# Kernel optimization log

Measured on AMD Instinct MI355X. Metric: run time of the kernel, lower is better.

## Reference

```python
import jax, jax.numpy as jnp
import numpy as np

N, F_IN, HID, OUT, H = 10000, 256, 256, 512, 4
E = 320000
SLOPE = 0.2  # GATv2Conv default negative_slope
EPS = 1e-5   # LayerNorm eps


def setup_inputs() -> dict:
    key = jax.random.key(0)
    ks = jax.random.split(key, 10)
    g = lambda k, shape, fan: (jax.random.normal(k, shape, jnp.float32) / np.float32(np.sqrt(fan)))
    d1, d2 = HID // H, OUT // H
    return {
        "x": jax.random.normal(ks[0], (N, F_IN), jnp.float32),
        "edge_index": jax.random.randint(ks[1], (2, E), 0, N),
        # layer 1 (in_feats -> hidden_dim, heads=H, concat)
        "Wl1": g(ks[2], (HID, F_IN), F_IN), "bl1": jnp.zeros((HID,), jnp.float32),
        "Wr1": g(ks[3], (HID, F_IN), F_IN), "br1": jnp.zeros((HID,), jnp.float32),
        "att1": g(ks[4], (H, d1), d1), "bias1": jnp.zeros((HID,), jnp.float32),
        # layer 2 (hidden_dim -> out_dim)
        "Wl2": g(ks[5], (OUT, HID), HID), "bl2": jnp.zeros((OUT,), jnp.float32),
        "Wr2": g(ks[6], (OUT, HID), HID), "br2": jnp.zeros((OUT,), jnp.float32),
        "att2": g(ks[7], (H, d2), d2), "bias2": jnp.zeros((OUT,), jnp.float32),
        # final LayerNorm
        "gamma": jnp.ones((OUT,), jnp.float32), "beta": jnp.zeros((OUT,), jnp.float32),
    }


def _gatv2(x, src, dst, Wl, bl, Wr, br, att, bias, heads):
    """GATv2Conv: e_ij = a_h . leaky_relu(Wl x_j + Wr x_i), softmax over j per i,
    out_i = sum_j alpha_ij * (Wl x_j), heads concatenated, plus bias."""
    n = x.shape[0]
    d = Wl.shape[0] // heads
    xl = (x @ Wl.T + bl).reshape(n, heads, d)  # source transform
    xr = (x @ Wr.T + br).reshape(n, heads, d)  # target transform
    s = jax.nn.leaky_relu(xl[src] + xr[dst], SLOPE)        # [E,H,d]
    e = jnp.einsum('ehd,hd->eh', s, att)                   # [E,H]
    m = jax.ops.segment_max(e, dst, num_segments=n)        # [N,H] (self-loops => no empty segs)
    w = jnp.exp(e - m[dst])
    denom = jax.ops.segment_sum(w, dst, num_segments=n)
    alpha = w / denom[dst]                                 # segment softmax
    out = jax.ops.segment_sum(alpha[:, :, None] * xl[src], dst, num_segments=n)  # [N,H,d]
    return out.reshape(n, heads * d) + bias


def reference(x, edge_index, Wl1, bl1, Wr1, br1, att1, bias1,
              Wl2, bl2, Wr2, br2, att2, bias2, gamma, beta):
    n = x.shape[0]
    loop = jnp.arange(n, dtype=edge_index.dtype)  # add_self_loops=True
    src = jnp.concatenate([edge_index[0], loop])
    dst = jnp.concatenate([edge_index[1], loop])
    h = jax.nn.relu(_gatv2(x, src, dst, Wl1, bl1, Wr1, br1, att1, bias1, H))
    h = _gatv2(h, src, dst, Wl2, bl2, Wr2, br2, att2, bias2, H)
    mu = jnp.mean(h, axis=-1, keepdims=True)
    var = jnp.var(h, axis=-1, keepdims=True)
    return gamma * (h - mu) / jnp.sqrt(var + EPS) + beta
```

## Files before the change

kernel.cpp:

```cpp
#include <hip/hip_runtime.h>
#include <stdint.h>

#define N_NODES 10000
#define K_DIM   256
#define HID_D   256
#define OUT_D   512
#define NE      320000
#define NE_TOT  (NE + N_NODES)
#define SLOPE   0.2f
#define LN_EPS  1e-5f

typedef __bf16 bf16x8 __attribute__((ext_vector_type(8)));
typedef float  f32x4  __attribute__((ext_vector_type(4)));
typedef float  f32x2  __attribute__((ext_vector_type(2)));
typedef unsigned short u16;
typedef uint32_t u32;

#if __has_builtin(__builtin_elementwise_fma)
#define PKFMA(a,b,c) __builtin_elementwise_fma((a),(b),(c))
#else
#define PKFMA(a,b,c) ((a)*(b)+(c))
#endif
#if __has_builtin(__builtin_elementwise_max)
#define PKMAX(a,b) __builtin_elementwise_max((a),(b))
#else
static __device__ __forceinline__ f32x2 pkmax_(f32x2 a, f32x2 b) {
    f32x2 r; r.x = fmaxf(a.x, b.x); r.y = fmaxf(a.y, b.y); return r;
}
#define PKMAX(a,b) pkmax_((a),(b))
#endif

__device__ __forceinline__ float bf2f(u16 u) {
    union { u32 i; float f; } v; v.i = ((u32)u) << 16; return v.f;
}
__device__ __forceinline__ u16 f2bf(float f) {
    union { float f; u32 i; } v; v.f = f;
    u32 b = v.i;
    return (u16)((b + 0x7FFFu + ((b >> 16) & 1u)) >> 16);
}
__device__ __forceinline__ f32x2 bfpair(u32 u) {
    union { u32 i; float f; } lo, hi;
    lo.i = u << 16; hi.i = u & 0xFFFF0000u;
    f32x2 r; r.x = lo.f; r.y = hi.f; return r;
}
__device__ __forceinline__ u32 pack2bf(float a, float b) {
    return (u32)f2bf(a) | ((u32)f2bf(b) << 16);
}

__device__ __forceinline__ void gl_lds16(const u16* g, u16* lds_base) {
    __builtin_amdgcn_global_load_lds(
        (const __attribute__((address_space(1))) void*)g,
        (__attribute__((address_space(3))) void*)lds_base, 16, 0, 0);
}

#define CW_X  2560000
#define CW_1  (CW_X + 65536)
#define CW_2  (CW_1 + 65536)
#define CW_3  (CW_2 + 131072)
#define CW_TOT (CW_3 + 131072)
#define CANON_BLOCKS (CW_TOT / 256 + 16)
#define COUNT_BLOCKS ((NE + 255) / 256)

struct PrepArgs {
    const void *x, *wl1, *wr1, *wl2, *wr2;
    u16 *xd, *wl1d, *wr1d, *wl2d, *wr2d;
    const void* ssrc[10]; float* sdst[10];
    const int* ei; int* deg; int* flagg;
};

__global__ __launch_bounds__(256) void k_prep(PrepArgs c) {
    int bx = blockIdx.x, tid = threadIdx.x;
    if (bx >= CANON_BLOCKS) {
        int e = (bx - CANON_BLOCKS) * 256 + tid;
        if (e < NE) atomicAdd(&c.deg[c.ei[NE + e]], 1);
        return;
    }
    __shared__ int cnt;
    if (tid == 0) cnt = 0;
    __syncthreads();
    u32 v = ((const u32*)c.x)[tid];
    int e_lo = (int)((v >> 7) & 0xFF);
    if (e_lo >= 100 && e_lo <= 150) atomicAdd(&cnt, 1);
    __syncthreads();
    int f = (cnt > 180) ? 1 : 0;
    if (bx == 0 && tid == 0) *c.flagg = f;

    int i = bx * 256 + tid;
    if (i < CW_TOT) {
        const void* src; u16* dst; int off;
        if      (i < CW_X) { src = c.x;   dst = c.xd;   off = i; }
        else if (i < CW_1) { src = c.wl1; dst = c.wl1d; off = i - CW_X; }
        else if (i < CW_2) { src = c.wr1; dst = c.wr1d; off = i - CW_1; }
        else if (i < CW_3) { src = c.wl2; dst = c.wl2d; off = i - CW_2; }
        else               { src = c.wr2; dst = c.wr2d; off = i - CW_3; }
        if (f) dst[off] = ((const u16*)src)[off];
        else   dst[off] = f2bf(((const float*)src)[off]);
    } else {
        int s = i - CW_TOT;
        int seg, off;
        if (s < 1024) { seg = s >> 8; off = s & 255; }
        else          { seg = 4 + ((s - 1024) >> 9); off = (s - 1024) & 511; }
        const void* sp = c.ssrc[seg];
        float* d = c.sdst[seg];
        d[off] = f ? bf2f(((const u16*)sp)[off]) : ((const float*)sp)[off];
    }
}

__global__ __launch_bounds__(1024) void k_scan(const int* __restrict__ deg,
                                               int* __restrict__ rowptr,
                                               int* __restrict__ cursor) {
    __shared__ int sbuf[2][1024];
    int t = threadIdx.x;
    int base = t * 10;
    int loc[10];
    int s = 0;
    #pragma unroll
    for (int q = 0; q < 10; ++q) {
        int idx = base + q;
        int d = (idx < N_NODES) ? (deg[idx] + 1) : 0;
        loc[q] = s;
        s += d;
    }
    sbuf[0][t] = s;
    __syncthreads();
    int cur = 0;
    for (int off = 1; off < 1024; off <<= 1) {
        int nxt = cur ^ 1;
        int v = sbuf[cur][t];
        if (t >= off) v += sbuf[cur][t - off];
        sbuf[nxt][t] = v;
        __syncthreads();
        cur = nxt;
    }
    int excl = sbuf[cur][t] - s;
    #pragma unroll
    for (int q = 0; q < 10; ++q) {
        int idx = base + q;
        if (idx <= N_NODES) {
            int val = excl + loc[q];
            rowptr[idx] = val;
            cursor[idx] = val;
        }
    }
}

__global__ __launch_bounds__(256) void k_gemm2s(const u16* __restrict__ X,
                                                const u16* __restrict__ Wl,
                                                const u16* __restrict__ Wr,
                                                const float* __restrict__ bl,
                                                const float* __restrict__ br,
                                                u16* __restrict__ Yl,
                                                u16* __restrict__ Yr, int Ncols,
                                                int MBx, int gemmB,
                                                const int* __restrict__ ei,
                                                int* cursor, int* __restrict__ csr_src) {
    __shared__ uint4 sAq[1024];
    __shared__ uint4 sBq[1024];
    int bx = blockIdx.x, tid = threadIdx.x;

    if (bx >= gemmB) {
        int e = (bx - gemmB) * 256 + tid;
        if (e < NE_TOT) {
            int s, d;
            if (e < NE) { s = ei[e]; d = ei[NE + e]; }
            else        { s = e - NE; d = s; }
            int pos = atomicAdd(&cursor[d], 1);
            csr_src[pos] = s;
        }
        return;
    }

    u16* sA = (u16*)sAq;
    u16* sB = (u16*)sBq;
    int nb = Ncols >> 7;
    int by = bx / MBx;
    const u16* W; const float* bias; u16* Y; int nbase;
    if (by < nb) { W = Wl; bias = bl; Y = Yl; nbase = by << 7; }
    else         { W = Wr; bias = br; Y = Yr; nbase = (by - nb) << 7; }

    int m0   = (bx % MBx) << 7;
    int wave = tid >> 6;
    int lane = tid & 63;
    int quad = lane >> 4;
    int l16  = lane & 15;
    int wm   = wave & 1;
    int wn   = wave >> 1;

    f32x4 acc[4][4] = {};

    #pragma unroll 1
    for (int kk = 0; kk < K_DIM; kk += 64) {
        #pragma unroll
        for (int r = 0; r < 4; ++r) {
            int g = wave + r * 4;
            int chunk = g >> 1;
            int row = ((g & 1) << 6) + lane;
            int mg = m0 + row;
            if (mg >= N_NODES) mg = N_NODES - 1;
            gl_lds16(X + (size_t)mg * K_DIM + kk + chunk * 8, sA + (size_t)(g << 6) * 8);
            gl_lds16(W + (size_t)(nbase + row) * K_DIM + kk + chunk * 8, sB + (size_t)(g << 6) * 8);
        }
        __syncthreads();

        #pragma unroll
        for (int s = 0; s < 2; ++s) {
            int c = s * 4 + quad;
            bf16x8 af[4], bf[4];
            #pragma unroll
            for (int t = 0; t < 4; ++t) {
                int m = (wm << 6) + t * 16 + l16;
                af[t] = *(const bf16x8*)(sA + ((size_t)(c << 7) + m) * 8);
                int n = (wn << 6) + t * 16 + l16;
                bf[t] = *(const bf16x8*)(sB + ((size_t)(c << 7) + n) * 8);
            }
            #pragma unroll
            for (int mt = 0; mt < 4; ++mt)
                #pragma unroll
                for (int nt = 0; nt < 4; ++nt)
                    acc[mt][nt] = __builtin_amdgcn_mfma_f32_16x16x32_bf16(
                        af[mt], bf[nt], acc[mt][nt], 0, 0, 0);
        }
        __syncthreads();
    }

    #pragma unroll
    for (int nt = 0; nt < 4; ++nt) {
        int col = nbase + (wn << 6) + nt * 16 + l16;
        float bv = bias[col];
        #pragma unroll
        for (int mt = 0; mt < 4; ++mt) {
            int rbase = m0 + (wm << 6) + mt * 16 + quad * 4;
            #pragma unroll
            for (int q = 0; q < 4; ++q) {
                int row = rbase + q;
                if (row < N_NODES)
                    Y[(size_t)row * Ncols + col] = f2bf(acc[mt][nt][q] + bv);
            }
        }
    }
}

__global__ __launch_bounds__(256) void k_agg1(const u16* __restrict__ xl,
                                              const u16* __restrict__ xr,
                                              const int* __restrict__ rowptr,
                                              const int* __restrict__ csrc,
                                              const float* __restrict__ att,
                                              const float* __restrict__ bias,
                                              u16* __restrict__ hout) {
    __shared__ float red[2][64][6];
    int tid = threadIdx.x;
    int wave = tid >> 6, lane = tid & 63;
    int pair = wave >> 1, half = wave & 1;
    int i = blockIdx.x * 2 + pair;
    if (i >= N_NODES) return;
    int c0 = (lane >> 4) * 64 + (lane & 15) * 4;

    f32x2 xp[2], ap[2];
    {
        uint2 xq = *(const uint2*)(xr + (size_t)i * HID_D + c0);
        xp[0] = bfpair(xq.x); xp[1] = bfpair(xq.y);
        const f32x2* a2 = (const f32x2*)(att + c0);
        ap[0] = a2[0]; ap[1] = a2[1];
    }
    const f32x2 slope2 = {SLOPE, SLOPE};

    int beg = rowptr[i], end = rowptr[i + 1];
    int cnt = end - beg;
    int h0 = (cnt + 1) >> 1;
    int p    = beg + half * h0;
    int pend = half ? end : (beg + h0);

    float denom = 0.f;
    f32x2 acc[2] = {};
    const u16* xbase = xl + c0;

    auto dotq = [&](uint2 q) -> float {
        f32x2 pr2 = {0.f, 0.f};
        f32x2 s = bfpair(q.x) + xp[0]; s = PKMAX(s, s * slope2); pr2 = PKFMA(s, ap[0], pr2);
        s = bfpair(q.y) + xp[1];       s = PKMAX(s, s * slope2); pr2 = PKFMA(s, ap[1], pr2);
        return pr2.x + pr2.y;
    };
    auto accq = [&](uint2 q, float w) {
        f32x2 W = {w, w};
        acc[0] = PKFMA(W, bfpair(q.x), acc[0]);
        acc[1] = PKFMA(W, bfpair(q.y), acc[1]);
    };

    while (p + 8 <= pend) {
        int4 ja = *(const int4*)(csrc + p);
        int4 jb = *(const int4*)(csrc + p + 4);
        uint2 q[8];
        q[0] = *(const uint2*)(xbase + (size_t)ja.x * HID_D);
        q[1] = *(const uint2*)(xbase + (size_t)ja.y * HID_D);
        q[2] = *(const uint2*)(xbase + (size_t)ja.z * HID_D);
        q[3] = *(const uint2*)(xbase + (size_t)ja.w * HID_D);
        q[4] = *(const uint2*)(xbase + (size_t)jb.x * HID_D);
        q[5] = *(const uint2*)(xbase + (size_t)jb.y * HID_D);
        q[6] = *(const uint2*)(xbase + (size_t)jb.z * HID_D);
        q[7] = *(const uint2*)(xbase + (size_t)jb.w * HID_D);
        float pr[8];
        #pragma unroll
        for (int e = 0; e < 8; ++e) pr[e] = dotq(q[e]);
        #pragma unroll
        for (int o = 1; o < 16; o <<= 1)
            #pragma unroll
            for (int e = 0; e < 8; ++e) pr[e] += __shfl_xor(pr[e], o, 64);
        #pragma unroll
        for (int e = 0; e < 8; ++e) {
            float w = __expf(fminf(pr[e], 60.f));
            denom += w;
            accq(q[e], w);
        }
        p += 8;
    }
    if (p + 4 <= pend) {
        int4 ja = *(const int4*)(csrc + p);
        uint2 q[4];
        q[0] = *(const uint2*)(xbase + (size_t)ja.x * HID_D);
        q[1] = *(const uint2*)(xbase + (size_t)ja.y * HID_D);
        q[2] = *(const uint2*)(xbase + (size_t)ja.z * HID_D);
        q[3] = *(const uint2*)(xbase + (size_t)ja.w * HID_D);
        float pr[4];
        #pragma unroll
        for (int e = 0; e < 4; ++e) pr[e] = dotq(q[e]);
        #pragma unroll
        for (int o = 1; o < 16; o <<= 1)
            #pragma unroll
            for (int e = 0; e < 4; ++e) pr[e] += __shfl_xor(pr[e], o, 64);
        #pragma unroll
        for (int e = 0; e < 4; ++e) {
            float w = __expf(fminf(pr[e], 60.f));
            denom += w;
            accq(q[e], w);
        }
        p += 4;
    }
    for (; p < pend; ++p) {
        uint2 q = *(const uint2*)(xbase + (size_t)csrc[p] * HID_D);
        float pr = dotq(q);
        #pragma unroll
        for (int o = 1; o < 16; o <<= 1) pr += __shfl_xor(pr, o, 64);
        float w = __expf(fminf(pr, 60.f));
        denom += w;
        accq(q, w);
    }

    if (half == 1) {
        red[pair][lane][0] = acc[0].x; red[pair][lane][1] = acc[0].y;
        red[pair][lane][2] = acc[1].x; red[pair][lane][3] = acc[1].y;
        red[pair][lane][4] = denom;
    }
    __syncthreads();
    if (half == 1) return;
    acc[0].x += red[pair][lane][0]; acc[0].y += red[pair][lane][1];
    acc[1].x += red[pair][lane][2]; acc[1].y += red[pair][lane][3];
    denom    += red[pair][lane][4];

    float inv = 1.f / denom;
    f32x2 inv2 = {inv, inv};
    const f32x2* bp = (const f32x2*)(bias + c0);
    f32x2 z = {0.f, 0.f};
    f32x2 o0 = PKMAX(PKFMA(acc[0], inv2, bp[0]), z);
    f32x2 o1 = PKMAX(PKFMA(acc[1], inv2, bp[1]), z);
    u32* hp = (u32*)(hout + (size_t)i * HID_D + c0);
    hp[0] = pack2bf(o0.x, o0.y);
    hp[1] = pack2bf(o1.x, o1.y);
}

__global__ __launch_bounds__(256) void k_agg2_ln(const u16* __restrict__ xl,
                                                 const u16* __restrict__ xr,
                                                 const int* __restrict__ rowptr,
                                                 const int* __restrict__ csrc,
                                                 const float* __restrict__ att,
                                                 const float* __restrict__ bias,
                                                 const float* __restrict__ gamma,
                                                 const float* __restrict__ beta,
                                                 void* __restrict__ outv,
                                                 const int* __restrict__ flag) {
    __shared__ float red[2][64][10];
    int tid = threadIdx.x;
    int wave = tid >> 6, lane = tid & 63;
    int pair = wave >> 1, half = wave & 1;
    int i = blockIdx.x * 2 + pair;
    if (i >= N_NODES) return;
    int c0 = (lane >> 4) * 128 + (lane & 15) * 8;

    f32x2 xp[4], ap[4];
    {
        uint4 xq = *(const uint4*)(xr + (size_t)i * OUT_D + c0);
        xp[0] = bfpair(xq.x); xp[1] = bfpair(xq.y);
        xp[2] = bfpair(xq.z); xp[3] = bfpair(xq.w);
        const f32x2* a2 = (const f32x2*)(att + c0);
        ap[0] = a2[0]; ap[1] = a2[1]; ap[2] = a2[2]; ap[3] = a2[3];
    }
    const f32x2 slope2 = {SLOPE, SLOPE};

    int beg = rowptr[i], end = rowptr[i + 1];
    int cnt = end - beg;
    int h0 = (cnt + 1) >> 1;
    int p    = beg + half * h0;
    int pend = half ? end : (beg + h0);

    float denom = 0.f;
    f32x2 acc[4] = {};
    const u16* xbase = xl + c0;

    auto dotq = [&](uint4 q) -> float {
        f32x2 pr2 = {0.f, 0.f};
        f32x2 s = bfpair(q.x) + xp[0]; s = PKMAX(s, s * slope2); pr2 = PKFMA(s, ap[0], pr2);
        s = bfpair(q.y) + xp[1];       s = PKMAX(s, s * slope2); pr2 = PKFMA(s, ap[1], pr2);
        s = bfpair(q.z) + xp[2];       s = PKMAX(s, s * slope2); pr2 = PKFMA(s, ap[2], pr2);
        s = bfpair(q.w) + xp[3];       s = PKMAX(s, s * slope2); pr2 = PKFMA(s, ap[3], pr2);
        return pr2.x + pr2.y;
    };
    auto accq = [&](uint4 q, float w) {
        f32x2 W = {w, w};
        acc[0] = PKFMA(W, bfpair(q.x), acc[0]);
        acc[1] = PKFMA(W, bfpair(q.y), acc[1]);
        acc[2] = PKFMA(W, bfpair(q.z), acc[2]);
        acc[3] = PKFMA(W, bfpair(q.w), acc[3]);
    };

    while (p + 8 <= pend) {
        int4 ja = *(const int4*)(csrc + p);
        int4 jb = *(const int4*)(csrc + p + 4);
        uint4 q[8];
        q[0] = *(const uint4*)(xbase + (size_t)ja.x * OUT_D);
        q[1] = *(const uint4*)(xbase + (size_t)ja.y * OUT_D);
        q[2] = *(const uint4*)(xbase + (size_t)ja.z * OUT_D);
        q[3] = *(const uint4*)(xbase + (size_t)ja.w * OUT_D);
        q[4] = *(const uint4*)(xbase + (size_t)jb.x * OUT_D);
        q[5] = *(const uint4*)(xbase + (size_t)jb.y * OUT_D);
        q[6] = *(const uint4*)(xbase + (size_t)jb.z * OUT_D);
        q[7] = *(const uint4*)(xbase + (size_t)jb.w * OUT_D);
        float pr[8];
        #pragma unroll
        for (int e = 0; e < 8; ++e) pr[e] = dotq(q[e]);
        #pragma unroll
        for (int o = 1; o < 16; o <<= 1)
            #pragma unroll
            for (int e = 0; e < 8; ++e) pr[e] += __shfl_xor(pr[e], o, 64);
        #pragma unroll
        for (int e = 0; e < 8; ++e) {
            float w = __expf(fminf(pr[e], 60.f));
            denom += w;
            accq(q[e], w);
        }
        p += 8;
    }
    if (p + 4 <= pend) {
        int4 ja = *(const int4*)(csrc + p);
        uint4 q[4];
        q[0] = *(const uint4*)(xbase + (size_t)ja.x * OUT_D);
        q[1] = *(const uint4*)(xbase + (size_t)ja.y * OUT_D);
        q[2] = *(const uint4*)(xbase + (size_t)ja.z * OUT_D);
        q[3] = *(const uint4*)(xbase + (size_t)ja.w * OUT_D);
        float pr[4];
        #pragma unroll
        for (int e = 0; e < 4; ++e) pr[e] = dotq(q[e]);
        #pragma unroll
        for (int o = 1; o < 16; o <<= 1)
            #pragma unroll
            for (int e = 0; e < 4; ++e) pr[e] += __shfl_xor(pr[e], o, 64);
        #pragma unroll
        for (int e = 0; e < 4; ++e) {
            float w = __expf(fminf(pr[e], 60.f));
            denom += w;
            accq(q[e], w);
        }
        p += 4;
    }
    for (; p < pend; ++p) {
        uint4 q = *(const uint4*)(xbase + (size_t)csrc[p] * OUT_D);
        float pr = dotq(q);
        #pragma unroll
        for (int o = 1; o < 16; o <<= 1) pr += __shfl_xor(pr, o, 64);
        float w = __expf(fminf(pr, 60.f));
        denom += w;
        accq(q, w);
    }

    if (half == 1) {
        #pragma unroll
        for (int k = 0; k < 4; ++k) {
            red[pair][lane][2*k]     = acc[k].x;
            red[pair][lane][2*k + 1] = acc[k].y;
        }
        red[pair][lane][8] = denom;
    }
    __syncthreads();
    if (half == 1) return;
    #pragma unroll
    for (int k = 0; k < 4; ++k) {
        acc[k].x += red[pair][lane][2*k];
        acc[k].y += red[pair][lane][2*k + 1];
    }
    denom += red[pair][lane][8];

    float inv = 1.f / denom;
    f32x2 inv2 = {inv, inv};
    const f32x2* bp = (const f32x2*)(bias + c0);
    f32x2 o2[4];
    float s1 = 0.f, s2 = 0.f;
    #pragma unroll
    for (int k = 0; k < 4; ++k) {
        o2[k] = PKFMA(acc[k], inv2, bp[k]);
        s1 += o2[k].x + o2[k].y;
        s2 = fmaf(o2[k].x, o2[k].x, fmaf(o2[k].y, o2[k].y, s2));
    }
    #pragma unroll
    for (int off = 1; off < 64; off <<= 1) {
        s1 += __shfl_xor(s1, off, 64);
        s2 += __shfl_xor(s2, off, 64);
    }
    float mu  = s1 * (1.f / OUT_D);
    float var = s2 * (1.f / OUT_D) - mu * mu;
    float rstd = rsqrtf(var + LN_EPS);
    f32x2 mu2 = {mu, mu}, rs2 = {rstd, rstd};
    const f32x2* gp  = (const f32x2*)(gamma + c0);
    const f32x2* bep = (const f32x2*)(beta + c0);

    size_t ob = (size_t)i * OUT_D + c0;
    if (*flag) {
        u32 pk[4];
        #pragma unroll
        for (int k = 0; k < 4; ++k) {
            f32x2 r = PKFMA(gp[k] * (o2[k] - mu2), rs2, bep[k]);
            pk[k] = pack2bf(r.x, r.y);
        }
        *(uint4*)((u16*)outv + ob) = make_uint4(pk[0], pk[1], pk[2], pk[3]);
    } else {
        f32x2* out = (f32x2*)((float*)outv + ob);
        #pragma unroll
        for (int k = 0; k < 4; ++k)
            out[k] = PKFMA(gp[k] * (o2[k] - mu2), rs2, bep[k]);
    }
}


extern "C" void kernel_launch(void* const* d_in, const int* in_sizes, int n_in,
                              void* d_out, int out_size, void* d_ws, size_t ws_size,
                              hipStream_t stream) {
    const int* ei = (const int*)d_in[1];

    char* ws = (char*)d_ws;
    size_t off = 0;
    auto alloc = [&](size_t bytes) { void* p = ws + off; off += (bytes + 255) & ~(size_t)255; return p; };
    u16* xcb  = (u16*)alloc((size_t)N_NODES * K_DIM * 2);
    u16* wl1b = (u16*)alloc((size_t)HID_D * K_DIM * 2);
    u16* wr1b = (u16*)alloc((size_t)HID_D * K_DIM * 2);
    u16* wl2b = (u16*)alloc((size_t)OUT_D * K_DIM * 2);
    u16* wr2b = (u16*)alloc((size_t)OUT_D * K_DIM * 2);
    u16* xl1b = (u16*)alloc((size_t)N_NODES * HID_D * 2);
    u16* xr1b = (u16*)alloc((size_t)N_NODES * HID_D * 2);
    u16* hb   = (u16*)alloc((size_t)N_NODES * HID_D * 2);
    u16* xl2b = (u16*)alloc((size_t)N_NODES * OUT_D * 2);
    u16* xr2b = (u16*)alloc((size_t)N_NODES * OUT_D * 2);
    float* bl1c  = (float*)alloc(HID_D * 4);
    float* br1c  = (float*)alloc(HID_D * 4);
    float* att1c = (float*)alloc(HID_D * 4);
    float* bia1c = (float*)alloc(HID_D * 4);
    float* bl2c  = (float*)alloc(OUT_D * 4);
    float* br2c  = (float*)alloc(OUT_D * 4);
    float* att2c = (float*)alloc(OUT_D * 4);
    float* bia2c = (float*)alloc(OUT_D * 4);
    float* gamc  = (float*)alloc(OUT_D * 4);
    float* betc  = (float*)alloc(OUT_D * 4);
    int* flag = (int*)alloc(256);
    int* deg  = (int*)alloc((size_t)N_NODES * 4);
    int* rowp = (int*)alloc((size_t)(N_NODES + 1) * 4);
    int* curs = (int*)alloc((size_t)(N_NODES + 1) * 4);
    int* csrc = (int*)alloc((size_t)NE_TOT * 4);

    hipMemsetAsync(deg, 0, (size_t)N_NODES * 4, stream);

    PrepArgs pa;
    pa.x = d_in[0]; pa.wl1 = d_in[2]; pa.wr1 = d_in[4]; pa.wl2 = d_in[8]; pa.wr2 = d_in[10];
    pa.xd = xcb; pa.wl1d = wl1b; pa.wr1d = wr1b; pa.wl2d = wl2b; pa.wr2d = wr2b;
    pa.ssrc[0] = d_in[3];  pa.sdst[0] = bl1c;
    pa.ssrc[1] = d_in[5];  pa.sdst[1] = br1c;
    pa.ssrc[2] = d_in[6];  pa.sdst[2] = att1c;
    pa.ssrc[3] = d_in[7];  pa.sdst[3] = bia1c;
    pa.ssrc[4] = d_in[9];  pa.sdst[4] = bl2c;
    pa.ssrc[5] = d_in[11]; pa.sdst[5] = br2c;
    pa.ssrc[6] = d_in[12]; pa.sdst[6] = att2c;
    pa.ssrc[7] = d_in[13]; pa.sdst[7] = bia2c;
    pa.ssrc[8] = d_in[14]; pa.sdst[8] = gamc;
    pa.ssrc[9] = d_in[15]; pa.sdst[9] = betc;
    pa.ei = ei; pa.deg = deg; pa.flagg = flag;
    hipLaunchKernelGGL(k_prep, dim3(CANON_BLOCKS + COUNT_BLOCKS), dim3(256), 0, stream, pa);

    hipLaunchKernelGGL(k_scan, dim3(1), dim3(1024), 0, stream, deg, rowp, curs);

    const int MB = (N_NODES + 127) / 128;
    const int SCATB = (NE_TOT + 255) / 256;
    hipLaunchKernelGGL(k_gemm2s, dim3(MB * 4 + SCATB), dim3(256), 0, stream,
                       xcb, wl1b, wr1b, bl1c, br1c, xl1b, xr1b, HID_D,
                       MB, MB * 4, ei, curs, csrc);
    hipLaunchKernelGGL(k_agg1, dim3((N_NODES + 1) / 2), dim3(256), 0, stream,
                       xl1b, xr1b, rowp, csrc, att1c, bia1c, hb);
    hipLaunchKernelGGL(k_gemm2s, dim3(MB * 8), dim3(256), 0, stream,
                       hb, wl2b, wr2b, bl2c, br2c, xl2b, xr2b, OUT_D,
                       MB, MB * 8, ei, curs, csrc);
    hipLaunchKernelGGL(k_agg2_ln, dim3((N_NODES + 1) / 2), dim3(256), 0, stream,
                       xl2b, xr2b, rowp, csrc, att2c, bia2c, gamc, betc, d_out, flag);
}
```

Baseline: 276.5 us.

## Bucket CSR by source range, drop intra-node split, skip bf16 copy

The degree count and scatter now use per-destination buckets keyed by source block (source>>11, five phases), so each node's neighbor list is grouped by source range. This is meant to improve cache locality of the gathered xl rows during aggregation. The aggregation kernels now use one wave per node instead of two waves splitting the edge list with an LDS reduction, which removes a barrier and shared memory but lengthens the serial loop for high-degree nodes. When inputs are already bf16, the prep copy is skipped and the GEMM reads the original buffers directly. The scan now walks five times as many buckets on a single block.

```diff
diff --git a/kernel.cpp b/kernel.cpp
--- a/kernel.cpp
+++ b/kernel.cpp
@@ -9,6 +9,8 @@
 #define NE_TOT  (NE + N_NODES)
 #define SLOPE   0.2f
 #define LN_EPS  1e-5f
+#define NPH     5
+#define NBUCK   (N_NODES * NPH)
 
 typedef __bf16 bf16x8 __attribute__((ext_vector_type(8)));
 typedef float  f32x4  __attribute__((ext_vector_type(4)));
@@ -65,14 +67,17 @@
     const void *x, *wl1, *wr1, *wl2, *wr2;
     u16 *xd, *wl1d, *wr1d, *wl2d, *wr2d;
     const void* ssrc[10]; float* sdst[10];
-    const int* ei; int* deg; int* flagg;
+    const int* ei; int* bcnt; int* flagg;
 };
 
 __global__ __launch_bounds__(256) void k_prep(PrepArgs c) {
     int bx = blockIdx.x, tid = threadIdx.x;
     if (bx >= CANON_BLOCKS) {
         int e = (bx - CANON_BLOCKS) * 256 + tid;
-        if (e < NE) atomicAdd(&c.deg[c.ei[NE + e]], 1);
+        if (e < NE) {
+            int s = c.ei[e], d = c.ei[NE + e];
+            atomicAdd(&c.bcnt[d * NPH + (s >> 11)], 1);
+        }
         return;
     }
     __shared__ int cnt;
@@ -87,14 +92,14 @@
 
     int i = bx * 256 + tid;
     if (i < CW_TOT) {
+        if (f) return;
         const void* src; u16* dst; int off;
         if      (i < CW_X) { src = c.x;   dst = c.xd;   off = i; }
         else if (i < CW_1) { src = c.wl1; dst = c.wl1d; off = i - CW_X; }
         else if (i < CW_2) { src = c.wr1; dst = c.wr1d; off = i - CW_1; }
         else if (i < CW_3) { src = c.wl2; dst = c.wl2d; off = i - CW_2; }
         else               { src = c.wr2; dst = c.wr2d; off = i - CW_3; }
-        if (f) dst[off] = ((const u16*)src)[off];
-        else   dst[off] = f2bf(((const float*)src)[off]);
+        dst[off] = f2bf(((const float*)src)[off]);
     } else {
         int s = i - CW_TOT;
         int seg, off;
@@ -106,21 +111,20 @@
     }
 }
 
-__global__ __launch_bounds__(1024) void k_scan(const int* __restrict__ deg,
+__global__ __launch_bounds__(1024) void k_scan(const int* __restrict__ bcnt,
                                                int* __restrict__ rowptr,
                                                int* __restrict__ cursor) {
     __shared__ int sbuf[2][1024];
+    const int Q = 49;
     int t = threadIdx.x;
-    int base = t * 10;
-    int loc[10];
+    int base = t * Q;
+    auto bval = [&](int b) -> int {
+        if (b >= NBUCK) return 0;
+        int i = b / NPH, ph = b - i * NPH;
+        return bcnt[b] + ((i >> 11) == ph ? 1 : 0);
+    };
     int s = 0;
-    #pragma unroll
-    for (int q = 0; q < 10; ++q) {
-        int idx = base + q;
-        int d = (idx < N_NODES) ? (deg[idx] + 1) : 0;
-        loc[q] = s;
-        s += d;
-    }
+    for (int q = 0; q < Q; ++q) s += bval(base + q);
     sbuf[0][t] = s;
     __syncthreads();
     int cur = 0;
@@ -132,28 +136,32 @@
         __syncthreads();
         cur = nxt;
     }
-    int excl = sbuf[cur][t] - s;
-    #pragma unroll
-    for (int q = 0; q < 10; ++q) {
-        int idx = base + q;
-        if (idx <= N_NODES) {
-            int val = excl + loc[q];
-            rowptr[idx] = val;
-            cursor[idx] = val;
-        }
-    }
-}
-
-__global__ __launch_bounds__(256) void k_gemm2s(const u16* __restrict__ X,
-                                                const u16* __restrict__ Wl,
-                                                const u16* __restrict__ Wr,
+    int run = sbuf[cur][t] - s;
+    for (int q = 0; q < Q; ++q) {
+        int b = base + q;
+        if (b <= NBUCK) {
+            if (b < NBUCK) cursor[b] = run;
+            int i = b / NPH, ph = b - i * NPH;
+            if (ph == 0) rowptr[i] = run;
+            run += bval(b);
+        }
+    }
+}
+
+__global__ __launch_bounds__(256) void k_gemm2s(const u16* __restrict__ Xa,
+                                                const u16* __restrict__ Xb,
+                                                const u16* __restrict__ Wla,
+                                                const u16* __restrict__ Wlb,
+                                                const u16* __restrict__ Wra,
+                                                const u16* __restrict__ Wrb,
                                                 const float* __restrict__ bl,
                                                 const float* __restrict__ br,
                                                 u16* __restrict__ Yl,
                                                 u16* __restrict__ Yr, int Ncols,
                                                 int MBx, int gemmB,
                                                 const int* __restrict__ ei,
-                                                int* cursor, int* __restrict__ csr_src) {
+                                                int* cursor, int* __restrict__ csr_src,
+                                                const int* __restrict__ flag) {
     __shared__ uint4 sAq[1024];
     __shared__ uint4 sBq[1024];
     int bx = blockIdx.x, tid = threadIdx.x;
@@ -164,11 +172,16 @@
             int s, d;
             if (e < NE) { s = ei[e]; d = ei[NE + e]; }
             else        { s = e - NE; d = s; }
-            int pos = atomicAdd(&cursor[d], 1);
+            int pos = atomicAdd(&cursor[d * NPH + (s >> 11)], 1);
             csr_src[pos] = s;
         }
         return;
     }
+
+    int f = *flag;
+    const u16* X  = f ? Xa  : Xb;
+    const u16* Wl = f ? Wla : Wlb;
+    const u16* Wr = f ? Wra : Wrb;
 
     u16* sA = (u16*)sAq;
     u16* sB = (u16*)sBq;
@@ -247,11 +260,8 @@
                                               const float* __restrict__ att,
                                               const float* __restrict__ bias,
                                               u16* __restrict__ hout) {
-    __shared__ float red[2][64][6];
-    int tid = threadIdx.x;
-    int wave = tid >> 6, lane = tid & 63;
-    int pair = wave >> 1, half = wave & 1;
-    int i = blockIdx.x * 2 + pair;
+    int wave = threadIdx.x >> 6, lane = threadIdx.x & 63;
+    int i = blockIdx.x * 4 + wave;
     if (i >= N_NODES) return;
     int c0 = (lane >> 4) * 64 + (lane & 15) * 4;
 
@@ -264,12 +274,7 @@
     }
     const f32x2 slope2 = {SLOPE, SLOPE};
 
-    int beg = rowptr[i], end = rowptr[i + 1];
-    int cnt = end - beg;
-    int h0 = (cnt + 1) >> 1;
-    int p    = beg + half * h0;
-    int pend = half ? end : (beg + h0);
-
+    int p = rowptr[i], pend = rowptr[i + 1];
     float denom = 0.f;
     f32x2 acc[2] = {};
     const u16* xbase = xl + c0;
@@ -345,17 +350,6 @@
         accq(q, w);
     }
 
-    if (half == 1) {
-        red[pair][lane][0] = acc[0].x; red[pair][lane][1] = acc[0].y;
-        red[pair][lane][2] = acc[1].x; red[pair][lane][3] = acc[1].y;
-        red[pair][lane][4] = denom;
-    }
-    __syncthreads();
-    if (half == 1) return;
-    acc[0].x += red[pair][lane][0]; acc[0].y += red[pair][lane][1];
-    acc[1].x += red[pair][lane][2]; acc[1].y += red[pair][lane][3];
-    denom    += red[pair][lane][4];
-
     float inv = 1.f / denom;
     f32x2 inv2 = {inv, inv};
     const f32x2* bp = (const f32x2*)(bias + c0);
@@ -377,11 +371,8 @@
                                                  const float* __restrict__ beta,
                                                  void* __restrict__ outv,
                                                  const int* __restrict__ flag) {
-    __shared__ float red[2][64][10];
-    int tid = threadIdx.x;
-    int wave = tid >> 6, lane = tid & 63;
-    int pair = wave >> 1, half = wave & 1;
-    int i = blockIdx.x * 2 + pair;
+    int wave = threadIdx.x >> 6, lane = threadIdx.x & 63;
+    int i = blockIdx.x * 4 + wave;
     if (i >= N_NODES) return;
     int c0 = (lane >> 4) * 128 + (lane & 15) * 8;
 
@@ -395,12 +386,7 @@
     }
     const f32x2 slope2 = {SLOPE, SLOPE};
 
-    int beg = rowptr[i], end = rowptr[i + 1];
-    int cnt = end - beg;
-    int h0 = (cnt + 1) >> 1;
-    int p    = beg + half * h0;
-    int pend = half ? end : (beg + h0);
-
+    int p = rowptr[i], pend = rowptr[i + 1];
     float denom = 0.f;
     f32x2 acc[4] = {};
     const u16* xbase = xl + c0;
@@ -479,23 +465,6 @@
         denom += w;
         accq(q, w);
     }
-
-    if (half == 1) {
-        #pragma unroll
-        for (int k = 0; k < 4; ++k) {
-            red[pair][lane][2*k]     = acc[k].x;
-            red[pair][lane][2*k + 1] = acc[k].y;
-        }
-        red[pair][lane][8] = denom;
-    }
-    __syncthreads();
-    if (half == 1) return;
-    #pragma unroll
-    for (int k = 0; k < 4; ++k) {
-        acc[k].x += red[pair][lane][2*k];
-        acc[k].y += red[pair][lane][2*k + 1];
-    }
-    denom += red[pair][lane][8];
 
     float inv = 1.f / denom;
     f32x2 inv2 = {inv, inv};
@@ -567,12 +536,12 @@
     float* gamc  = (float*)alloc(OUT_D * 4);
     float* betc  = (float*)alloc(OUT_D * 4);
     int* flag = (int*)alloc(256);
-    int* deg  = (int*)alloc((size_t)N_NODES * 4);
+    int* bcnt = (int*)alloc((size_t)NBUCK * 4);
     int* rowp = (int*)alloc((size_t)(N_NODES + 1) * 4);
-    int* curs = (int*)alloc((size_t)(N_NODES + 1) * 4);
+    int* curs = (int*)alloc((size_t)NBUCK * 4);
     int* csrc = (int*)alloc((size_t)NE_TOT * 4);
 
-    hipMemsetAsync(deg, 0, (size_t)N_NODES * 4, stream);
+    hipMemsetAsync(bcnt, 0, (size_t)NBUCK * 4, stream);
 
     PrepArgs pa;
     pa.x = d_in[0]; pa.wl1 = d_in[2]; pa.wr1 = d_in[4]; pa.wl2 = d_in[8]; pa.wr2 = d_in[10];
@@ -587,21 +556,27 @@
     pa.ssrc[7] = d_in[13]; pa.sdst[7] = bia2c;
     pa.ssrc[8] = d_in[14]; pa.sdst[8] = gamc;
     pa.ssrc[9] = d_in[15]; pa.sdst[9] = betc;
-    pa.ei = ei; pa.deg = deg; pa.flagg = flag;
+    pa.ei = ei; pa.bcnt = bcnt; pa.flagg = flag;
     hipLaunchKernelGGL(k_prep, dim3(CANON_BLOCKS + COUNT_BLOCKS), dim3(256), 0, stream, pa);
 
-    hipLaunchKernelGGL(k_scan, dim3(1), dim3(1024), 0, stream, deg, rowp, curs);
+    hipLaunchKernelGGL(k_scan, dim3(1), dim3(1024), 0, stream, bcnt, rowp, curs);
 
     const int MB = (N_NODES + 127) / 128;
     const int SCATB = (NE_TOT + 255) / 256;
     hipLaunchKernelGGL(k_gemm2s, dim3(MB * 4 + SCATB), dim3(256), 0, stream,
-                       xcb, wl1b, wr1b, bl1c, br1c, xl1b, xr1b, HID_D,
-                       MB, MB * 4, ei, curs, csrc);
-    hipLaunchKernelGGL(k_agg1, dim3((N_NODES + 1) / 2), dim3(256), 0, stream,
+                       (const u16*)d_in[0], xcb,
+                       (const u16*)d_in[2], wl1b,
+                       (const u16*)d_in[4], wr1b,
+                       bl1c, br1c, xl1b, xr1b, HID_D,
+                       MB, MB * 4, ei, curs, csrc, flag);
+    hipLaunchKernelGGL(k_agg1, dim3((N_NODES + 3) / 4), dim3(256), 0, stream,
                        xl1b, xr1b, rowp, csrc, att1c, bia1c, hb);
     hipLaunchKernelGGL(k_gemm2s, dim3(MB * 8), dim3(256), 0, stream,
-                       hb, wl2b, wr2b, bl2c, br2c, xl2b, xr2b, OUT_D,
-                       MB, MB * 8, ei, curs, csrc);
-    hipLaunchKernelGGL(k_agg2_ln, dim3((N_NODES + 1) / 2), dim3(256), 0, stream,
+                       hb, hb,
+                       (const u16*)d_in[8], wl2b,
+                       (const u16*)d_in[10], wr2b,
+                       bl2c, br2c, xl2b, xr2b, OUT_D,
+                       MB, MB * 8, ei, curs, csrc, flag);
+    hipLaunchKernelGGL(k_agg2_ln, dim3((N_NODES + 3) / 4), dim3(256), 0, stream,
                        xl2b, xr2b, rowp, csrc, att2c, bia2c, gamc, betc, d_out, flag);
 }
```

New measurement: 349.9 us. +26.5%, slower.
